# Optimization experiments

Measured on AMD Instinct MI355X. Metric: run time of the kernel, lower is better.

## Reference

```python
import jax, jax.numpy as jnp
import numpy as np

LN_EPS = 1e-5

def _layer_norm(x, w, b):
    m = jnp.mean(x, axis=-1, keepdims=True)
    v = jnp.mean(jnp.square(x - m), axis=-1, keepdims=True)
    return (x - m) * jax.lax.rsqrt(v + LN_EPS) * w + b

def setup_inputs() -> dict:
    key = jax.random.key(0)
    ks = jax.random.split(key, 6)
    B, T, D, H = 64, 512, 512, 512
    x = jax.random.normal(ks[0], (B, T, D), dtype=jnp.float32)
    h = jax.random.normal(ks[1], (B, H), dtype=jnp.float32)
    # orthogonal-ish init approximated by scaled normal (math-equivalent shapes)
    w_ih = jax.random.normal(ks[2], (3 * H, D), dtype=jnp.float32) / np.sqrt(D)
    b_ih = jnp.zeros((3 * H,), dtype=jnp.float32)
    w_hh = jax.random.normal(ks[3], (3 * H, H), dtype=jnp.float32) / np.sqrt(H)
    b_hh = jnp.zeros((3 * H,), dtype=jnp.float32)
    ln_r_w = jnp.ones((H,), jnp.float32); ln_r_b = jnp.zeros((H,), jnp.float32)
    ln_z_w = jnp.ones((H,), jnp.float32); ln_z_b = jnp.zeros((H,), jnp.float32)
    ln_n_w = jnp.ones((H,), jnp.float32); ln_n_b = jnp.zeros((H,), jnp.float32)
    return dict(x=x, h=h, w_ih=w_ih, b_ih=b_ih, w_hh=w_hh, b_hh=b_hh,
                ln_r_w=ln_r_w, ln_r_b=ln_r_b, ln_z_w=ln_z_w, ln_z_b=ln_z_b,
                ln_n_w=ln_n_w, ln_n_b=ln_n_b)

def reference(x, h, w_ih, b_ih, w_hh, b_hh, ln_r_w, ln_r_b, ln_z_w, ln_z_b, ln_n_w, ln_n_b):
    H = h.shape[-1]
    # precompute input gate projections for all timesteps: [B, T, 3H] -> [T, B, 3H]
    x_gates_all = jnp.einsum('btd,gd->btg', x, w_ih) + b_ih
    x_gates_all = jnp.swapaxes(x_gates_all, 0, 1)

    def step(h, x_gates):
        h_gates = jnp.matmul(h, w_hh.T) + b_hh
        x_r, x_z, x_n = jnp.split(x_gates, 3, axis=-1)
        h_r, h_z, h_n = jnp.split(h_gates, 3, axis=-1)
        r = jax.nn.sigmoid(_layer_norm(x_r + h_r, ln_r_w, ln_r_b))
        z = jax.nn.sigmoid(_layer_norm(x_z + h_z, ln_z_w, ln_z_b))
        n = jnp.tanh(_layer_norm(x_n + r * h_n, ln_n_w, ln_n_b))
        h_new = (1.0 - z) * n + z * h
        return h_new, h_new

    h_last, out_tbh = jax.lax.scan(step, h, x_gates_all)
    out = jnp.swapaxes(out_tbh, 0, 1)  # [B, T, H]
    return out, h_last
```

## Files before the change

kernel.cpp:

```cpp
#include <hip/hip_runtime.h>
#include <hip/hip_bf16.h>

#define B_ 64
#define T_ 512
#define D_ 512
#define H_ 512
#define G3 1536
#define NBLK 16

typedef float f32x4 __attribute__((ext_vector_type(4)));
typedef __bf16 bf16x8 __attribute__((ext_vector_type(8)));
typedef unsigned long long qword;

#define LDSP 56
#define WPITCH 520

union bfpack { bf16x8 v; __hip_bfloat16 h[8]; };
union q2bf { qword q[2]; bf16x8 v; };
union qf2  { qword q; float f[2]; };
union qbf4 { qword q; __hip_bfloat16 h[4]; };

__device__ inline bf16x8 cvt8(const float* __restrict__ p) {
    float4 f0 = *(const float4*)p;
    float4 f1 = *(const float4*)(p + 4);
    bfpack u;
    u.h[0] = __float2bfloat16(f0.x); u.h[1] = __float2bfloat16(f0.y);
    u.h[2] = __float2bfloat16(f0.z); u.h[3] = __float2bfloat16(f0.w);
    u.h[4] = __float2bfloat16(f1.x); u.h[5] = __float2bfloat16(f1.y);
    u.h[6] = __float2bfloat16(f1.z); u.h[7] = __float2bfloat16(f1.w);
    return u.v;
}

__device__ inline qword ld_coh(const qword* p) {
    return __hip_atomic_load(p, __ATOMIC_RELAXED, __HIP_MEMORY_SCOPE_AGENT);
}
__device__ inline void st_coh(float* p, float v) {
    __hip_atomic_store(p, v, __ATOMIC_RELAXED, __HIP_MEMORY_SCOPE_AGENT);
}
__device__ inline void st_coh64(qword* p, qword v) {
    __hip_atomic_store(p, v, __ATOMIC_RELAXED, __HIP_MEMORY_SCOPE_AGENT);
}

__device__ inline void barrier_slot(unsigned int* ctr, int slot) {
    __hip_atomic_fetch_add(&ctr[slot], 1u, __ATOMIC_RELAXED, __HIP_MEMORY_SCOPE_AGENT);
    int spins = 0;
    while (__hip_atomic_load(&ctr[slot], __ATOMIC_RELAXED, __HIP_MEMORY_SCOPE_AGENT) < NBLK) {
        if (++spins > (1 << 22)) { spins = 0; __threadfence(); }
    }
}

__global__ void k0_init(const float* __restrict__ h_in,
                        __hip_bfloat16* __restrict__ hb,
                        unsigned int* __restrict__ ctr) {
    int i = blockIdx.x * blockDim.x + threadIdx.x;
    if (i < B_ * H_) hb[i] = __float2bfloat16(h_in[i]);
    if (i < 1024)    ctr[i] = 0u;
}

__global__ __launch_bounds__(256) void k1_xgemm(
    const float* __restrict__ X, const float* __restrict__ W,
    const float* __restrict__ bias, __hip_bfloat16* __restrict__ XG)
{
    __shared__ __align__(16) __hip_bfloat16 la[128 * LDSP];
    __shared__ __align__(16) __hip_bfloat16 lb[128 * LDSP];
    int tid = threadIdx.x, bx = blockIdx.x;
    int m0 = (bx / 12) * 128, n0 = (bx % 12) * 128;
    int wave = tid >> 6, lane = tid & 63;
    int wh = wave >> 1, ww = wave & 1;
    int l15 = lane & 15, kq = lane >> 4;

    f32x4 acc[4][4];
    #pragma unroll
    for (int i = 0; i < 4; i++)
        #pragma unroll
        for (int j = 0; j < 4; j++) acc[i][j] = (f32x4){0.f, 0.f, 0.f, 0.f};

    for (int kt = 0; kt < 16; ++kt) {
        int k0 = kt * 32;
        for (int s = tid; s < 512; s += 256) {
            int r = s >> 2, c = s & 3;
            *(bf16x8*)&la[r * LDSP + c * 8] = cvt8(&X[(size_t)(m0 + r) * D_ + k0 + c * 8]);
            *(bf16x8*)&lb[r * LDSP + c * 8] = cvt8(&W[(size_t)(n0 + r) * D_ + k0 + c * 8]);
        }
        __syncthreads();
        bf16x8 af[4], bq[4];
        #pragma unroll
        for (int i = 0; i < 4; i++)
            af[i] = *(const bf16x8*)&la[(wh * 64 + i * 16 + l15) * LDSP + kq * 8];
        #pragma unroll
        for (int j = 0; j < 4; j++)
            bq[j] = *(const bf16x8*)&lb[(ww * 64 + j * 16 + l15) * LDSP + kq * 8];
        #pragma unroll
        for (int i = 0; i < 4; i++)
            #pragma unroll
            for (int j = 0; j < 4; j++)
                acc[i][j] = __builtin_amdgcn_mfma_f32_16x16x32_bf16(af[i], bq[j], acc[i][j], 0, 0, 0);
        __syncthreads();
    }
    #pragma unroll
    for (int i = 0; i < 4; i++)
        #pragma unroll
        for (int j = 0; j < 4; j++)
            #pragma unroll
            for (int r = 0; r < 4; r++) {
                int m = m0 + wh * 64 + i * 16 + kq * 4 + r;
                int n = n0 + ww * 64 + j * 16 + l15;
                int b = m >> 9, t = m & 511;
                XG[((size_t)t * B_ + b) * G3 + n] = __float2bfloat16(acc[i][j][r] + bias[n]);
            }
}

__global__ __launch_bounds__(512, 1) void k2_recur(
    const float* __restrict__ h_in, const float* __restrict__ Whh,
    const float* __restrict__ b_hh,
    const float* __restrict__ lnrw, const float* __restrict__ lnrb,
    const float* __restrict__ lnzw, const float* __restrict__ lnzb,
    const float* __restrict__ lnnw, const float* __restrict__ lnnb,
    const __hip_bfloat16* __restrict__ XG,
    float* __restrict__ HG, __hip_bfloat16* __restrict__ HB,
    unsigned int* __restrict__ ctr, float* __restrict__ out)
{
    __shared__ __align__(16) __hip_bfloat16 lw[96 * WPITCH];
    __shared__ float sc[32];

    const int tid = threadIdx.x;
    const int blk = blockIdx.x;
    const int n0 = blk * 96;
    const int s0 = blk * 4;

    for (int idx = tid; idx < 96 * 64; idx += 512) {
        int row = idx >> 6, ch = idx & 63;
        *(bf16x8*)&lw[row * WPITCH + ch * 8] = cvt8(&Whh[(size_t)(n0 + row) * H_ + ch * 8]);
    }

    const int w = tid >> 6, lane = tid & 63;
    const int l15 = lane & 15, kq = lane >> 4;
    const int mt = w >> 1;
    const int nj0 = (w & 1) * 3;

    const int sid = tid >> 7;
    const int c = tid & 127;
    const int b = s0 + sid;

    float bhr[4], bhz[4], bhn[4], wr[4], br_[4], wz[4], bz_[4], wn[4], bn_[4], hf[4];
    #pragma unroll
    for (int j = 0; j < 4; j++) {
        int col = 4 * c + j;
        bhr[j] = b_hh[col];       bhz[j] = b_hh[512 + col]; bhn[j] = b_hh[1024 + col];
        wr[j] = lnrw[col]; br_[j] = lnrb[col];
        wz[j] = lnzw[col]; bz_[j] = lnzb[col];
        wn[j] = lnnw[col]; bn_[j] = lnnb[col];
        hf[j] = h_in[b * H_ + col];
    }
    __syncthreads();

    const float inv = 1.0f / 512.0f;
    const qword* hbq_base = (const qword*)HB + (size_t)(mt * 16 + l15) * 128 + kq * 2;
    const float* hg_mine = HG + (size_t)b * G3 + 4 * c;

    for (int t = 0; t < T_; ++t) {
        const qword* xgq = (const qword*)(XG + ((size_t)t * B_ + b) * G3) + c;
        qbf4 xr8, xz8, xn8;
        xr8.q = xgq[0];
        xz8.q = xgq[128];
        xn8.q = xgq[256];

        q2bf afr[16];
        #pragma unroll
        for (int kt = 0; kt < 16; kt++) {
            afr[kt].q[0] = ld_coh(hbq_base + kt * 8);
            afr[kt].q[1] = ld_coh(hbq_base + kt * 8 + 1);
        }
        f32x4 a0 = {0,0,0,0}, a1 = {0,0,0,0}, a2 = {0,0,0,0};
        #pragma unroll
        for (int kt = 0; kt < 16; kt++) {
            bf16x8 b0 = *(const bf16x8*)&lw[((nj0    ) * 16 + l15) * WPITCH + kt * 32 + kq * 8];
            bf16x8 b1 = *(const bf16x8*)&lw[((nj0 + 1) * 16 + l15) * WPITCH + kt * 32 + kq * 8];
            bf16x8 b2 = *(const bf16x8*)&lw[((nj0 + 2) * 16 + l15) * WPITCH + kt * 32 + kq * 8];
            a0 = __builtin_amdgcn_mfma_f32_16x16x32_bf16(afr[kt].v, b0, a0, 0, 0, 0);
            a1 = __builtin_amdgcn_mfma_f32_16x16x32_bf16(afr[kt].v, b1, a1, 0, 0, 0);
            a2 = __builtin_amdgcn_mfma_f32_16x16x32_bf16(afr[kt].v, b2, a2, 0, 0, 0);
        }
        {
            int rowb = mt * 16 + kq * 4;
            int colb = n0 + nj0 * 16 + l15;
            #pragma unroll
            for (int r = 0; r < 4; r++) {
                st_coh(&HG[(rowb + r) * G3 + colb     ], a0[r]);
                st_coh(&HG[(rowb + r) * G3 + colb + 16], a1[r]);
                st_coh(&HG[(rowb + r) * G3 + colb + 32], a2[r]);
            }
        }
        asm volatile("s_waitcnt vmcnt(0)" ::: "memory");
        __syncthreads();
        if (tid == 0) barrier_slot(ctr, 2 * t);
        __syncthreads();

        qf2 hr01, hr23, hz01, hz23, hn01, hn23;
        hr01.q = ld_coh((const qword*)(hg_mine));
        hr23.q = ld_coh((const qword*)(hg_mine + 2));
        hz01.q = ld_coh((const qword*)(hg_mine + 512));
        hz23.q = ld_coh((const qword*)(hg_mine + 514));
        hn01.q = ld_coh((const qword*)(hg_mine + 1024));
        hn23.q = ld_coh((const qword*)(hg_mine + 1026));
        float hgr[4]  = {hr01.f[0], hr01.f[1], hr23.f[0], hr23.f[1]};
        float hgz[4]  = {hz01.f[0], hz01.f[1], hz23.f[0], hz23.f[1]};
        float hgnv[4] = {hn01.f[0], hn01.f[1], hn23.f[0], hn23.f[1]};

        float ar[4], az[4], hgn[4], xn[4];
        float sr = 0.f, ssr = 0.f, sz = 0.f, ssz = 0.f;
        #pragma unroll
        for (int j = 0; j < 4; j++) {
            ar[j]  = __bfloat162float(xr8.h[j]) + hgr[j] + bhr[j];
            az[j]  = __bfloat162float(xz8.h[j]) + hgz[j] + bhz[j];
            hgn[j] = hgnv[j] + bhn[j];
            xn[j]  = __bfloat162float(xn8.h[j]);
            sr += ar[j]; ssr += ar[j] * ar[j];
            sz += az[j]; ssz += az[j] * az[j];
        }
        #pragma unroll
        for (int off = 32; off; off >>= 1) {
            sr += __shfl_down(sr, off); ssr += __shfl_down(ssr, off);
            sz += __shfl_down(sz, off); ssz += __shfl_down(ssz, off);
        }
        if (lane == 0) { sc[w * 4] = sr; sc[w * 4 + 1] = ssr; sc[w * 4 + 2] = sz; sc[w * 4 + 3] = ssz; }
        __syncthreads();
        {
            int w0 = sid * 2;
            sr  = sc[w0 * 4]     + sc[(w0 + 1) * 4];
            ssr = sc[w0 * 4 + 1] + sc[(w0 + 1) * 4 + 1];
            sz  = sc[w0 * 4 + 2] + sc[(w0 + 1) * 4 + 2];
            ssz = sc[w0 * 4 + 3] + sc[(w0 + 1) * 4 + 3];
        }
        __syncthreads();
        float mr = sr * inv, vr = ssr * inv - mr * mr, rstd_r = rsqrtf(vr + 1e-5f);
        float mz = sz * inv, vz = ssz * inv - mz * mz, rstd_z = rsqrtf(vz + 1e-5f);
        float rg[4], zg[4], an[4];
        float sn = 0.f, ssn = 0.f;
        #pragma unroll
        for (int j = 0; j < 4; j++) {
            rg[j] = 1.f / (1.f + __expf(-((ar[j] - mr) * rstd_r * wr[j] + br_[j])));
            zg[j] = 1.f / (1.f + __expf(-((az[j] - mz) * rstd_z * wz[j] + bz_[j])));
            an[j] = xn[j] + rg[j] * hgn[j];
            sn += an[j]; ssn += an[j] * an[j];
        }
        #pragma unroll
        for (int off = 32; off; off >>= 1) {
            sn += __shfl_down(sn, off); ssn += __shfl_down(ssn, off);
        }
        if (lane == 0) { sc[w * 4] = sn; sc[w * 4 + 1] = ssn; }
        __syncthreads();
        {
            int w0 = sid * 2;
            sn  = sc[w0 * 4]     + sc[(w0 + 1) * 4];
            ssn = sc[w0 * 4 + 1] + sc[(w0 + 1) * 4 + 1];
        }
        __syncthreads();
        float mn = sn * inv, vn = ssn * inv - mn * mn, rstd_n = rsqrtf(vn + 1e-5f);
        float hnew[4];
        qbf4 hbnew;
        #pragma unroll
        for (int j = 0; j < 4; j++) {
            float ng = tanhf((an[j] - mn) * rstd_n * wn[j] + bn_[j]);
            hnew[j] = (1.f - zg[j]) * ng + zg[j] * hf[j];
            hf[j] = hnew[j];
            hbnew.h[j] = __float2bfloat16(hnew[j]);
        }
        st_coh64((qword*)HB + (size_t)b * 128 + c, hbnew.q);
        asm volatile("s_waitcnt vmcnt(0)" ::: "memory");
        __syncthreads();
        if (tid == 0) barrier_slot(ctr, 2 * t + 1);
        __syncthreads();
        *(f32x4*)(out + ((size_t)b * T_ + t) * H_ + 4 * c) =
            (f32x4){hnew[0], hnew[1], hnew[2], hnew[3]};
        if (t == T_ - 1) {
            *(f32x4*)(out + (size_t)B_ * T_ * H_ + b * H_ + 4 * c) =
                (f32x4){hnew[0], hnew[1], hnew[2], hnew[3]};
        }
    }
}

extern "C" void kernel_launch(void* const* d_in, const int* in_sizes, int n_in,
                              void* d_out, int out_size, void* d_ws, size_t ws_size,
                              hipStream_t stream)
{
    const float* x    = (const float*)d_in[0];
    const float* h    = (const float*)d_in[1];
    const float* w_ih = (const float*)d_in[2];
    const float* b_ih = (const float*)d_in[3];
    const float* w_hh = (const float*)d_in[4];
    const float* b_hh = (const float*)d_in[5];
    const float* lnrw = (const float*)d_in[6];
    const float* lnrb = (const float*)d_in[7];
    const float* lnzw = (const float*)d_in[8];
    const float* lnzb = (const float*)d_in[9];
    const float* lnnw = (const float*)d_in[10];
    const float* lnnb = (const float*)d_in[11];
    float* out = (float*)d_out;

    char* ws = (char*)d_ws;
    __hip_bfloat16* XG = (__hip_bfloat16*)ws;
    float*          HG = (float*)(ws + 100663296);
    __hip_bfloat16* HB = (__hip_bfloat16*)(ws + 101056512);
    unsigned int*  CTR = (unsigned int*)(ws + 101122048);

    k0_init<<<128, 256, 0, stream>>>(h, HB, CTR);
    k1_xgemm<<<3072, 256, 0, stream>>>(x, w_ih, b_ih, XG);
    k2_recur<<<NBLK, 512, 0, stream>>>(h, w_hh, b_hh,
        lnrw, lnrb, lnzw, lnzb, lnnw, lnnb, XG, HG, HB, CTR, out);
}
```

Before: 6.931 ms.

## Replace grid barriers with tagged data flags and per-block step flags

Drops the two atomic-counter grid barriers per timestep. Each h-gate value pair is now packed as bf16 together with a step tag in one 64-bit word, so consumers spin until the tag matches instead of waiting on a barrier. The second barrier becomes per-block progress flags that the 16 lanes poll before reading h. This is meant to cut synchronisation latency on the serial recurrence, at the cost of rounding the h-gate GEMM outputs to bf16 and of extra shuffles and spin-polling traffic.

```diff
diff --git a/kernel.cpp b/kernel.cpp
--- a/kernel.cpp
+++ b/kernel.cpp
@@ -17,7 +17,6 @@
 
 union bfpack { bf16x8 v; __hip_bfloat16 h[8]; };
 union q2bf { qword q[2]; bf16x8 v; };
-union qf2  { qword q; float f[2]; };
 union qbf4 { qword q; __hip_bfloat16 h[4]; };
 
 __device__ inline bf16x8 cvt8(const float* __restrict__ p) {
@@ -34,27 +33,40 @@
 __device__ inline qword ld_coh(const qword* p) {
     return __hip_atomic_load(p, __ATOMIC_RELAXED, __HIP_MEMORY_SCOPE_AGENT);
 }
-__device__ inline void st_coh(float* p, float v) {
-    __hip_atomic_store(p, v, __ATOMIC_RELAXED, __HIP_MEMORY_SCOPE_AGENT);
+__device__ inline unsigned int ld_coh32(const unsigned int* p) {
+    return __hip_atomic_load(p, __ATOMIC_RELAXED, __HIP_MEMORY_SCOPE_AGENT);
 }
 __device__ inline void st_coh64(qword* p, qword v) {
     __hip_atomic_store(p, v, __ATOMIC_RELAXED, __HIP_MEMORY_SCOPE_AGENT);
 }
-
-__device__ inline void barrier_slot(unsigned int* ctr, int slot) {
-    __hip_atomic_fetch_add(&ctr[slot], 1u, __ATOMIC_RELAXED, __HIP_MEMORY_SCOPE_AGENT);
-    int spins = 0;
-    while (__hip_atomic_load(&ctr[slot], __ATOMIC_RELAXED, __HIP_MEMORY_SCOPE_AGENT) < NBLK) {
-        if (++spins > (1 << 22)) { spins = 0; __threadfence(); }
-    }
+__device__ inline void st_coh32(unsigned int* p, unsigned int v) {
+    __hip_atomic_store(p, v, __ATOMIC_RELAXED, __HIP_MEMORY_SCOPE_AGENT);
+}
+
+__device__ inline qword pack_hg(float a, float b, unsigned int tag) {
+    union { __hip_bfloat16 h; unsigned short u; } ua, ub;
+    ua.h = __float2bfloat16(a); ub.h = __float2bfloat16(b);
+    return (qword)((unsigned int)ua.u | ((unsigned int)ub.u << 16)) | ((qword)tag << 32);
+}
+__device__ inline float hg_lo(qword q) {
+    union { unsigned short u; __hip_bfloat16 h; } x;
+    x.u = (unsigned short)(q & 0xffffu);
+    return __bfloat162float(x.h);
+}
+__device__ inline float hg_hi(qword q) {
+    union { unsigned short u; __hip_bfloat16 h; } x;
+    x.u = (unsigned short)((q >> 16) & 0xffffu);
+    return __bfloat162float(x.h);
 }
 
 __global__ void k0_init(const float* __restrict__ h_in,
                         __hip_bfloat16* __restrict__ hb,
-                        unsigned int* __restrict__ ctr) {
+                        qword* __restrict__ hgp,
+                        unsigned int* __restrict__ flags) {
     int i = blockIdx.x * blockDim.x + threadIdx.x;
     if (i < B_ * H_) hb[i] = __float2bfloat16(h_in[i]);
-    if (i < 1024)    ctr[i] = 0u;
+    for (int k = i; k < 64 * 768; k += 32768) hgp[k] = 0ull;
+    if (i < NBLK) flags[i] = 1u;
 }
 
 __global__ __launch_bounds__(256) void k1_xgemm(
@@ -117,8 +129,8 @@
     const float* __restrict__ lnzw, const float* __restrict__ lnzb,
     const float* __restrict__ lnnw, const float* __restrict__ lnnb,
     const __hip_bfloat16* __restrict__ XG,
-    float* __restrict__ HG, __hip_bfloat16* __restrict__ HB,
-    unsigned int* __restrict__ ctr, float* __restrict__ out)
+    qword* __restrict__ HGP, __hip_bfloat16* __restrict__ HB,
+    unsigned int* __restrict__ flags, float* __restrict__ out)
 {
     __shared__ __align__(16) __hip_bfloat16 lw[96 * WPITCH];
     __shared__ float sc[32];
@@ -137,6 +149,7 @@
     const int l15 = lane & 15, kq = lane >> 4;
     const int mt = w >> 1;
     const int nj0 = (w & 1) * 3;
+    const bool evenl = (l15 & 1) == 0;
 
     const int sid = tid >> 7;
     const int c = tid & 127;
@@ -156,14 +169,25 @@
 
     const float inv = 1.0f / 512.0f;
     const qword* hbq_base = (const qword*)HB + (size_t)(mt * 16 + l15) * 128 + kq * 2;
-    const float* hg_mine = HG + (size_t)b * G3 + 4 * c;
+    const qword* hg_mine = HGP + (size_t)b * 768 + 2 * c;
 
     for (int t = 0; t < T_; ++t) {
+        const unsigned int tag = (unsigned int)(t + 1);
+
         const qword* xgq = (const qword*)(XG + ((size_t)t * B_ + b) * G3) + c;
         qbf4 xr8, xz8, xn8;
         xr8.q = xgq[0];
         xz8.q = xgq[128];
         xn8.q = xgq[256];
+
+        {
+            int spins = 0;
+            for (;;) {
+                unsigned int f = ld_coh32(&flags[lane & 15]);
+                if (__all((int)(f >= tag))) break;
+                if (++spins > (1 << 18)) { spins = 0; __threadfence(); }
+            }
+        }
 
         q2bf afr[16];
         #pragma unroll
@@ -186,26 +210,39 @@
             int colb = n0 + nj0 * 16 + l15;
             #pragma unroll
             for (int r = 0; r < 4; r++) {
-                st_coh(&HG[(rowb + r) * G3 + colb     ], a0[r]);
-                st_coh(&HG[(rowb + r) * G3 + colb + 16], a1[r]);
-                st_coh(&HG[(rowb + r) * G3 + colb + 32], a2[r]);
+                float o0 = a0[r], o1 = a1[r], o2 = a2[r];
+                float p0 = __shfl_xor(o0, 1);
+                float p1 = __shfl_xor(o1, 1);
+                float p2 = __shfl_xor(o2, 1);
+                if (evenl) {
+                    qword* rowp = HGP + (size_t)(rowb + r) * 768;
+                    st_coh64(rowp + ((colb     ) >> 1), pack_hg(o0, p0, tag));
+                    st_coh64(rowp + ((colb + 16) >> 1), pack_hg(o1, p1, tag));
+                    st_coh64(rowp + ((colb + 32) >> 1), pack_hg(o2, p2, tag));
+                }
             }
         }
-        asm volatile("s_waitcnt vmcnt(0)" ::: "memory");
-        __syncthreads();
-        if (tid == 0) barrier_slot(ctr, 2 * t);
-        __syncthreads();
-
-        qf2 hr01, hr23, hz01, hz23, hn01, hn23;
-        hr01.q = ld_coh((const qword*)(hg_mine));
-        hr23.q = ld_coh((const qword*)(hg_mine + 2));
-        hz01.q = ld_coh((const qword*)(hg_mine + 512));
-        hz23.q = ld_coh((const qword*)(hg_mine + 514));
-        hn01.q = ld_coh((const qword*)(hg_mine + 1024));
-        hn23.q = ld_coh((const qword*)(hg_mine + 1026));
-        float hgr[4]  = {hr01.f[0], hr01.f[1], hr23.f[0], hr23.f[1]};
-        float hgz[4]  = {hz01.f[0], hz01.f[1], hz23.f[0], hz23.f[1]};
-        float hgnv[4] = {hn01.f[0], hn01.f[1], hn23.f[0], hn23.f[1]};
+
+        qword qr0, qr1, qz0, qz1, qn0, qn1;
+        {
+            int spins = 0;
+            for (;;) {
+                qr0 = ld_coh(hg_mine);           qr1 = ld_coh(hg_mine + 1);
+                qz0 = ld_coh(hg_mine + 256);     qz1 = ld_coh(hg_mine + 257);
+                qn0 = ld_coh(hg_mine + 512);     qn1 = ld_coh(hg_mine + 513);
+                bool ok = ((unsigned int)(qr0 >> 32) == tag) &
+                          ((unsigned int)(qr1 >> 32) == tag) &
+                          ((unsigned int)(qz0 >> 32) == tag) &
+                          ((unsigned int)(qz1 >> 32) == tag) &
+                          ((unsigned int)(qn0 >> 32) == tag) &
+                          ((unsigned int)(qn1 >> 32) == tag);
+                if (ok) break;
+                if (++spins > (1 << 18)) { spins = 0; __threadfence(); }
+            }
+        }
+        float hgr[4]  = {hg_lo(qr0), hg_hi(qr0), hg_lo(qr1), hg_hi(qr1)};
+        float hgz[4]  = {hg_lo(qz0), hg_hi(qz0), hg_lo(qz1), hg_hi(qz1)};
+        float hgnv[4] = {hg_lo(qn0), hg_hi(qn0), hg_lo(qn1), hg_hi(qn1)};
 
         float ar[4], az[4], hgn[4], xn[4];
         float sr = 0.f, ssr = 0.f, sz = 0.f, ssz = 0.f;
@@ -269,8 +306,7 @@
         st_coh64((qword*)HB + (size_t)b * 128 + c, hbnew.q);
         asm volatile("s_waitcnt vmcnt(0)" ::: "memory");
         __syncthreads();
-        if (tid == 0) barrier_slot(ctr, 2 * t + 1);
-        __syncthreads();
+        if (tid == 0) st_coh32(&flags[blk], (unsigned int)(t + 2));
         *(f32x4*)(out + ((size_t)b * T_ + t) * H_ + 4 * c) =
             (f32x4){hnew[0], hnew[1], hnew[2], hnew[3]};
         if (t == T_ - 1) {
@@ -300,12 +336,12 @@
 
     char* ws = (char*)d_ws;
     __hip_bfloat16* XG = (__hip_bfloat16*)ws;
-    float*          HG = (float*)(ws + 100663296);
+    qword*         HGP = (qword*)(ws + 100663296);
     __hip_bfloat16* HB = (__hip_bfloat16*)(ws + 101056512);
-    unsigned int*  CTR = (unsigned int*)(ws + 101122048);
-
-    k0_init<<<128, 256, 0, stream>>>(h, HB, CTR);
+    unsigned int*  FLG = (unsigned int*)(ws + 101122048);
+
+    k0_init<<<128, 256, 0, stream>>>(h, HB, HGP, FLG);
     k1_xgemm<<<3072, 256, 0, stream>>>(x, w_ih, b_ih, XG);
     k2_recur<<<NBLK, 512, 0, stream>>>(h, w_hh, b_hh,
-        lnrw, lnrb, lnzw, lnzb, lnnw, lnnb, XG, HG, HB, CTR, out);
-}
+        lnrw, lnrb, lnzw, lnzb, lnnw, lnnb, XG, HGP, HB, FLG, out);
+}
```

Result: slower. 7.564 ms (+9.1%).
